# Kernel tuning notes

Hardware: AMD Instinct MI355X
Metric: run time of the kernel (lower is better)

Reference implementation:

```python
import jax, jax.numpy as jnp
import numpy as np

K = 64          # channels
B, D, H, W = 1, 64, 64, 64
W_STD = 1.0 / np.sqrt(K * 9)  # kaiming-like scale for 3x3 conv, fan_in = K*3*3


def _conv2d(x, w):
    # x: [B, C, A1, A2], w: [O, I, 3, 3]; SAME padding, stride 1, no bias
    return jax.lax.conv_general_dilated(
        x, w, window_strides=(1, 1), padding=((1, 1), (1, 1)),
        dimension_numbers=("NCHW", "OIHW", "NCHW"))


def _spatial_pass(x, w, tdim, reverse):
    # x: [B, C, D, H, W]; scan over tensor dim `tdim` (2=D, 3=H, 4=W).
    # Each slice (size-1 kernel along tdim in the original Conv3d) reduces to a
    # 2D 3x3 conv over the remaining two spatial axes.
    xs = jnp.moveaxis(x, tdim, 0)              # [L, B, C, A1, A2]
    if reverse:
        xs = xs[::-1]
    y0 = xs[0]

    def step(carry, sl):
        y = sl + jax.nn.relu(_conv2d(carry, w))
        return y, y

    _, ys = jax.lax.scan(step, y0, xs[1:])
    ys = jnp.concatenate([y0[None], ys], axis=0)
    if reverse:
        ys = ys[::-1]
    return jnp.moveaxis(ys, 0, tdim)


def setup_inputs() -> dict:
    key = jax.random.key(0)
    ks = jax.random.split(key, 7)
    x = jax.random.normal(ks[0], (B, K, D, H, W), dtype=jnp.float32)
    mk = lambda k: (jax.random.normal(k, (K, K, 3, 3), dtype=jnp.float32) * W_STD)
    # 2D equivalents of the six Conv3d weights (size-1 kernel axis squeezed):
    #   up_down/down_up:    (3,1,3) -> 3x3 over (D,W), scan over H
    #   left_right/right_left: (3,3,1) -> 3x3 over (D,H), scan over W
    #   front_back/back_front: (1,3,3) -> 3x3 over (H,W), scan over D
    return {
        "x": x,
        "w_ud": mk(ks[1]), "w_du": mk(ks[2]),
        "w_lr": mk(ks[3]), "w_rl": mk(ks[4]),
        "w_fb": mk(ks[5]), "w_bf": mk(ks[6]),
    }


def reference(x, w_ud, w_du, w_lr, w_rl, w_fb, w_bf):
    # dims = [1,1,2,2,0,0] in spatial coords -> tensor dims [3,3,4,4,2,2]
    x = _spatial_pass(x, w_ud, 3, False)
    x = _spatial_pass(x, w_du, 3, True)
    x = _spatial_pass(x, w_lr, 4, False)
    x = _spatial_pass(x, w_rl, 4, True)
    x = _spatial_pass(x, w_fb, 2, False)
    x = _spatial_pass(x, w_bf, 2, True)
    return x
```

## Files before the change

kernel.cpp:

```cpp
#include <hip/hip_runtime.h>

#define NELEM     16777216
#define CI_STRIDE 262144
#define WTP_PASS  36864
#define NFLAG     (6 * 256 * 16)
#define EX_PAR    262144

__device__ float    g_bufA[NELEM + 32];
__device__ float    g_bufB[NELEM + 32];
__device__ float    g_wtp[6 * WTP_PASS];
__device__ float    g_exch[2 * EX_PAR];
__device__ unsigned g_flags[NFLAG];

static __device__ __forceinline__ float ald(const float* p) {
    return __hip_atomic_load(p, __ATOMIC_RELAXED, __HIP_MEMORY_SCOPE_AGENT);
}
static __device__ __forceinline__ void ast(float* p, float v) {
    __hip_atomic_store(p, v, __ATOMIC_RELAXED, __HIP_MEMORY_SCOPE_AGENT);
}
static __device__ __forceinline__ float g4(const float4 v, int i) {
    switch (i) { case 0: return v.x; case 1: return v.y;
                 case 2: return v.z; default: return v.w; }
}

static __device__ __forceinline__ void kmap(int k, int& row, int& col) {
    if      (k < 4)  { row = 0;    col = k;      }
    else if (k < 8)  { row = 5;    col = k - 4;  }
    else if (k < 12) { row = k-7;  col = 0;      }
    else if (k < 16) { row = k-11; col = 5;      }
    else if (k < 18) { row = 0;    col = k - 12; }
    else             { row = 5;    col = k - 14; }
}

__global__ __launch_bounds__(256) void prep(
    const float* __restrict__ w0, const float* __restrict__ w1,
    const float* __restrict__ w2, const float* __restrict__ w3,
    const float* __restrict__ w4, const float* __restrict__ w5)
{
    int gid = blockIdx.x * 256 + threadIdx.x;
    if (gid < NFLAG) g_flags[gid] = 0;
    if (gid >= 6 * WTP_PASS) return;
    int p  = gid / WTP_PASS;
    int r  = gid % WTP_PASS;
    int co = r & 63;
    int q  = r >> 6;
    int kx = q % 3;
    int t2 = q / 3;
    int ky = t2 % 3;
    int ci = t2 / 3;
    const float* src = (p==0)?w0:(p==1)?w1:(p==2)?w2:(p==3)?w3:(p==4)?w4:w5;
    g_wtp[gid] = (p < 4) ? src[co*576 + ci*9 + ky*3 + kx]
                         : src[co*576 + ci*9 + kx*3 + ky];
}

__global__ __launch_bounds__(256) void transpose_hw(
    const float* __restrict__ in, float* __restrict__ out)
{
    __shared__ float t[64][65];
    const size_t base = (size_t)blockIdx.x * 4096;
    const int c  = threadIdx.x & 63;
    const int r4 = threadIdx.x >> 6;
#pragma unroll
    for (int r = 0; r < 16; ++r) {
        int a = r4 * 16 + r;
        t[a][c] = in[base + a * 64 + c];
    }
    __syncthreads();
#pragma unroll
    for (int r = 0; r < 16; ++r) {
        int bb = r4 * 16 + r;
        out[base + (size_t)bb * 64 + c] = t[c][bb];
    }
}

__global__ __launch_bounds__(512, 2) void pass_kernel(
    float* __restrict__ buf, const float* __restrict__ wtp,
    unsigned* __restrict__ flags, float* __restrict__ exch,
    int st, int su, int dir)
{
    __shared__ float lds[21504];
    float* rint = lds;
    float* ring = lds + 1024;
    float* red  = lds + 2560;

    const int tid  = threadIdx.x;
    const int lane = tid & 63;
    const int wv   = tid >> 6;
    const int B  = blockIdx.x;
    const int bu = ((B & 7) << 1) | ((B >> 7) & 1);
    const int bv = (B >> 3) & 15;
    const int b  = bu * 16 + bv;
    const int u0 = bu << 2, v0 = bv << 2;
    const int rr = wv >> 1, cc0 = (wv & 1) << 1;
    const int p0 = wv << 1;

    float W[8][3][3];
#pragma unroll
    for (int i = 0; i < 8; ++i)
#pragma unroll
        for (int ky = 0; ky < 3; ++ky)
#pragma unroll
            for (int kx = 0; kx < 3; ++kx)
                W[i][ky][kx] = wtp[(((wv*8 + i)*3 + ky)*3 + kx)*64 + lane];

    int nbr = -1;
    if (lane < 8) {
        int c  = lane + (lane >= 4 ? 1 : 0);
        int nu = bu + c/3 - 1, nv = bv + c%3 - 1;
        if (nu >= 0 && nu < 16 && nv >= 0 && nv < 16) nbr = (nu*16 + nv)*16;
    }

    int kk0=-1, kk1=-1, kk2=-1, so0=0, so1=0, so2=0;
#pragma unroll
    for (int j = 0; j < 3; ++j) {
        int k = wv + 8*j;
        if (k >= 20) continue;
        int row, col; kmap(k, row, col);
        int du = (row==0)?-1:(row==5)?1:0, dv = (col==0)?-1:(col==5)?1:0;
        int nu = bu + du, nv = bv + dv;
        if (nu < 0 || nu > 15 || nv < 0 || nv > 15) continue;
        int nb = nu*16 + nv;
        int lr = (row==0)?3:(row==5)?0:row-1;
        int lc = (col==0)?3:(col==5)?0:col-1;
        int so = (nb*16 + lr*4 + lc)*64 + lane;
        if      (j == 0) { kk0 = k; so0 = so; }
        else if (j == 1) { kk1 = k; so1 = so; }
        else             { kk2 = k; so2 = so; }
    }

    const int t0 = (dir > 0) ? 0 : 63;
    {
        const float2 iv = *(const float2*)(buf + (size_t)t0*st
              + (size_t)lane*CI_STRIDE + (size_t)(u0+rr)*su + (v0+cc0));
        *(float2*)&rint[(rr*64 + lane)*4 + cc0] = iv;
    }
#pragma unroll
    for (int j = 0; j < 3; ++j) {
        int k = wv + 8*j;
        if (k >= 20) continue;
        int row, col; kmap(k, row, col);
        int gu = u0 - 1 + row, gv = v0 - 1 + col;
        float v = 0.f;
        if (gu >= 0 && gu < 64 && gv >= 0 && gv < 64)
            v = buf[(size_t)t0*st + (size_t)lane*CI_STRIDE + (size_t)gu*su + gv];
        ring[lane*24 + k] = v;
    }
    __syncthreads();

    for (int s = 1; s <= 63; ++s) {
        const int t = (dir > 0) ? s : 63 - s;

        if (wv == 0 && s > 1) {
            const unsigned tgt = (unsigned)(s - 1);
            bool ok = (nbr < 0);
            if (!ok) ok = __hip_atomic_load(&flags[nbr], __ATOMIC_RELAXED,
                                            __HIP_MEMORY_SCOPE_AGENT) >= tgt;
            int spins = 0;
            while (!__all(ok) && spins < (1 << 22)) {
                __builtin_amdgcn_s_sleep(1);
                if (!ok) ok = __hip_atomic_load(&flags[nbr], __ATOMIC_RELAXED,
                                                __HIP_MEMORY_SCOPE_AGENT) >= tgt;
                ++spins;
            }
        }
        __syncthreads();

        const float2 xv = *(const float2*)(buf + (size_t)t*st
              + (size_t)lane*CI_STRIDE + (size_t)(u0+rr)*su + (v0+cc0));

        float c0 = 0.f, c1 = 0.f, c2 = 0.f;
        if (s > 1) {
            const float* xsrc = exch + (size_t)((s-1) & 1) * EX_PAR;
            if (kk0 >= 0) c0 = ald(xsrc + so0);
            if (kk1 >= 0) c1 = ald(xsrc + so1);
            if (kk2 >= 0) c2 = ald(xsrc + so2);
        }

        float acc[16];
#pragma unroll
        for (int p = 0; p < 16; ++p) acc[p] = 0.f;

#pragma unroll
        for (int i = 0; i < 8; ++i) {
            const int ci = wv*8 + i;
            const float4 R0 = *(const float4*)&rint[(0*64 + ci)*4];
            const float4 R1 = *(const float4*)&rint[(1*64 + ci)*4];
            const float4 R2 = *(const float4*)&rint[(2*64 + ci)*4];
            const float4 R3 = *(const float4*)&rint[(3*64 + ci)*4];
#pragma unroll
            for (int oi = 0; oi < 4; ++oi)
#pragma unroll
            for (int ky = 0; ky < 3; ++ky) {
                const int wr = oi + ky;
                if (wr < 1 || wr > 4) continue;
                const float4 Rw = (wr==1)?R0:(wr==2)?R1:(wr==3)?R2:R3;
#pragma unroll
                for (int oj = 0; oj < 4; ++oj)
#pragma unroll
                for (int kx = 0; kx < 3; ++kx) {
                    const int wc = oj + kx;
                    if (wc < 1 || wc > 4) continue;
                    acc[oi*4+oj] = fmaf(W[i][ky][kx], g4(Rw, wc-1), acc[oi*4+oj]);
                }
            }
        }

        if (s > 1) {
            if (kk0 >= 0) ring[lane*24 + kk0] = c0;
            if (kk1 >= 0) ring[lane*24 + kk1] = c1;
            if (kk2 >= 0) ring[lane*24 + kk2] = c2;
        }
        __syncthreads();

#pragma unroll
        for (int i = 0; i < 8; ++i) {
            const int ci = wv*8 + i;
            const float4 r0a = *(const float4*)&ring[ci*24 + 0];
            const float4 r5a = *(const float4*)&ring[ci*24 + 4];
            const float4 cl  = *(const float4*)&ring[ci*24 + 8];
            const float4 cr  = *(const float4*)&ring[ci*24 + 12];
            const float2 r0b = *(const float2*)&ring[ci*24 + 16];
            const float2 r5b = *(const float2*)&ring[ci*24 + 18];
#pragma unroll
            for (int oi = 0; oi < 4; ++oi)
#pragma unroll
            for (int ky = 0; ky < 3; ++ky) {
                const int wr = oi + ky;
#pragma unroll
                for (int oj = 0; oj < 4; ++oj)
#pragma unroll
                for (int kx = 0; kx < 3; ++kx) {
                    const int wc = oj + kx;
                    if (wr >= 1 && wr <= 4 && wc >= 1 && wc <= 4) continue;
                    float cell;
                    if      (wr == 0) cell = (wc < 4) ? g4(r0a, wc)
                                             : (wc == 4 ? r0b.x : r0b.y);
                    else if (wr == 5) cell = (wc < 4) ? g4(r5a, wc)
                                             : (wc == 4 ? r5b.x : r5b.y);
                    else if (wc == 0) cell = g4(cl, wr-1);
                    else              cell = g4(cr, wr-1);
                    acc[oi*4+oj] = fmaf(W[i][ky][kx], cell, acc[oi*4+oj]);
                }
            }
        }

#pragma unroll
        for (int p = 0; p < 16; ++p)
            red[(wv*16 + p)*64 + lane] = acc[p];
        __syncthreads();

        float s0 = 0.f, s1 = 0.f;
#pragma unroll
        for (int g = 0; g < 8; ++g) {
            s0 += red[(g*16 + p0    )*64 + lane];
            s1 += red[(g*16 + p0 + 1)*64 + lane];
        }
        const float o0 = xv.x + fmaxf(s0, 0.f);
        const float o1 = xv.y + fmaxf(s1, 0.f);

        *(float2*)(buf + (size_t)t*st + (size_t)lane*CI_STRIDE
                   + (size_t)(u0+rr)*su + (v0+cc0)) = make_float2(o0, o1);
        if (s < 63) {
            *(float2*)&rint[(rr*64 + lane)*4 + cc0] = make_float2(o0, o1);
            float* eb = exch + (size_t)(s & 1)*EX_PAR + b*1024;
            ast(eb + (p0    )*64 + lane, o0);
            ast(eb + (p0 + 1)*64 + lane, o1);
        }
        __syncthreads();

        if (s < 63 && tid == 0)
            __hip_atomic_store(&flags[b*16], (unsigned)s, __ATOMIC_RELAXED,
                               __HIP_MEMORY_SCOPE_AGENT);
    }
}

extern "C" void kernel_launch(void* const* d_in, const int* in_sizes, int n_in,
                              void* d_out, int out_size, void* d_ws, size_t ws_size,
                              hipStream_t stream)
{
    (void)in_sizes; (void)n_in; (void)out_size; (void)d_ws; (void)ws_size;
    const float* x = (const float*)d_in[0];
    float* out = (float*)d_out;

    void *pa, *pb, *pw, *pf, *pe;
    hipGetSymbolAddress(&pa, HIP_SYMBOL(g_bufA));
    hipGetSymbolAddress(&pb, HIP_SYMBOL(g_bufB));
    hipGetSymbolAddress(&pw, HIP_SYMBOL(g_wtp));
    hipGetSymbolAddress(&pf, HIP_SYMBOL(g_flags));
    hipGetSymbolAddress(&pe, HIP_SYMBOL(g_exch));
    float* A  = (float*)pa + 16;
    float* Bb = (float*)pb + 16;
    float* wtp = (float*)pw;
    unsigned* flags = (unsigned*)pf;
    float* exch = (float*)pe;

    prep<<<864, 256, 0, stream>>>(
        (const float*)d_in[1], (const float*)d_in[2], (const float*)d_in[3],
        (const float*)d_in[4], (const float*)d_in[5], (const float*)d_in[6]);

    hipMemcpyAsync(A, x, (size_t)NELEM * sizeof(float),
                   hipMemcpyDeviceToDevice, stream);

    pass_kernel<<<256, 512, 0, stream>>>(A, wtp + 0*WTP_PASS, flags + 0*4096, exch, 64, 4096, +1);
    pass_kernel<<<256, 512, 0, stream>>>(A, wtp + 1*WTP_PASS, flags + 1*4096, exch, 64, 4096, -1);

    transpose_hw<<<4096, 256, 0, stream>>>(A, Bb);

    pass_kernel<<<256, 512, 0, stream>>>(Bb, wtp + 2*WTP_PASS, flags + 2*4096, exch, 64, 4096, +1);
    pass_kernel<<<256, 512, 0, stream>>>(Bb, wtp + 3*WTP_PASS, flags + 3*4096, exch, 64, 4096, -1);
    pass_kernel<<<256, 512, 0, stream>>>(Bb, wtp + 4*WTP_PASS, flags + 4*4096, exch, 4096, 64, +1);
    pass_kernel<<<256, 512, 0, stream>>>(Bb, wtp + 5*WTP_PASS, flags + 5*4096, exch, 4096, 64, -1);

    transpose_hw<<<4096, 256, 0, stream>>>(Bb, out);
}
```

Baseline: 2.490 ms.

## Switch to channels-last layout and double pass-kernel block size to 1024 threads

Replaces the channel-major layout with a channels-last buffer, so each of the 64 channels at a spatial point is contiguous. The input memcpy and mid transpose become one relayout kernel at entry and one at exit, and the pass kernel takes three strides so one layout serves all six scan directions. Pass-kernel blocks grow from 512 to 1024 threads, with each wave computing half the output rows of its channel group. The intent is fully coalesced per-step loads and stores and more parallelism per step. The cost is more LDS reduction traffic per step and higher register and occupancy pressure from launch_bounds(1024,4).

```diff
diff --git a/kernel.cpp b/kernel.cpp
--- a/kernel.cpp
+++ b/kernel.cpp
@@ -1,13 +1,11 @@
 #include <hip/hip_runtime.h>
 
 #define NELEM     16777216
-#define CI_STRIDE 262144
 #define WTP_PASS  36864
 #define NFLAG     (6 * 256 * 16)
 #define EX_PAR    262144
 
-__device__ float    g_bufA[NELEM + 32];
-__device__ float    g_bufB[NELEM + 32];
+__device__ float    g_bufA[NELEM];
 __device__ float    g_wtp[6 * WTP_PASS];
 __device__ float    g_exch[2 * EX_PAR];
 __device__ unsigned g_flags[NFLAG];
@@ -49,34 +47,53 @@
     int ky = t2 % 3;
     int ci = t2 / 3;
     const float* src = (p==0)?w0:(p==1)?w1:(p==2)?w2:(p==3)?w3:(p==4)?w4:w5;
-    g_wtp[gid] = (p < 4) ? src[co*576 + ci*9 + ky*3 + kx]
-                         : src[co*576 + ci*9 + kx*3 + ky];
-}
-
-__global__ __launch_bounds__(256) void transpose_hw(
+    g_wtp[gid] = src[co*576 + ci*9 + ky*3 + kx];
+}
+
+__global__ __launch_bounds__(256) void relayout_in(
     const float* __restrict__ in, float* __restrict__ out)
 {
     __shared__ float t[64][65];
-    const size_t base = (size_t)blockIdx.x * 4096;
+    const int o = blockIdx.x;
     const int c  = threadIdx.x & 63;
     const int r4 = threadIdx.x >> 6;
 #pragma unroll
     for (int r = 0; r < 16; ++r) {
-        int a = r4 * 16 + r;
-        t[a][c] = in[base + a * 64 + c];
+        int ch = r4 * 16 + r;
+        t[ch][c] = in[(size_t)ch * 262144 + o * 64 + c];
     }
     __syncthreads();
 #pragma unroll
     for (int r = 0; r < 16; ++r) {
-        int bb = r4 * 16 + r;
-        out[base + (size_t)bb * 64 + c] = t[c][bb];
-    }
-}
-
-__global__ __launch_bounds__(512, 2) void pass_kernel(
+        int j = r4 * 16 + r;
+        out[((size_t)o * 64 + j) * 64 + c] = t[c][j];
+    }
+}
+
+__global__ __launch_bounds__(256) void relayout_out(
+    const float* __restrict__ in, float* __restrict__ out)
+{
+    __shared__ float t[64][65];
+    const int o = blockIdx.x;
+    const int c  = threadIdx.x & 63;
+    const int r4 = threadIdx.x >> 6;
+#pragma unroll
+    for (int r = 0; r < 16; ++r) {
+        int j = r4 * 16 + r;
+        t[j][c] = in[((size_t)o * 64 + j) * 64 + c];
+    }
+    __syncthreads();
+#pragma unroll
+    for (int r = 0; r < 16; ++r) {
+        int ch = r4 * 16 + r;
+        out[(size_t)ch * 262144 + o * 64 + c] = t[c][ch];
+    }
+}
+
+__global__ __launch_bounds__(1024, 4) void pass_kernel(
     float* __restrict__ buf, const float* __restrict__ wtp,
     unsigned* __restrict__ flags, float* __restrict__ exch,
-    int st, int su, int dir)
+    int stp, int sup, int svp, int dir)
 {
     __shared__ float lds[21504];
     float* rint = lds;
@@ -86,13 +103,15 @@
     const int tid  = threadIdx.x;
     const int lane = tid & 63;
     const int wv   = tid >> 6;
+    const int g    = wv & 7;
+    const int h    = wv >> 3;
+    const int oiB  = 2 * h;
     const int B  = blockIdx.x;
     const int bu = ((B & 7) << 1) | ((B >> 7) & 1);
     const int bv = (B >> 3) & 15;
     const int b  = bu * 16 + bv;
     const int u0 = bu << 2, v0 = bv << 2;
-    const int rr = wv >> 1, cc0 = (wv & 1) << 1;
-    const int p0 = wv << 1;
+    const int row = wv >> 2, col = wv & 3;
 
     float W[8][3][3];
 #pragma unroll
@@ -101,7 +120,7 @@
         for (int ky = 0; ky < 3; ++ky)
 #pragma unroll
             for (int kx = 0; kx < 3; ++kx)
-                W[i][ky][kx] = wtp[(((wv*8 + i)*3 + ky)*3 + kx)*64 + lane];
+                W[i][ky][kx] = wtp[(((g*8 + i)*3 + ky)*3 + kx)*64 + lane];
 
     int nbr = -1;
     if (lane < 8) {
@@ -110,39 +129,34 @@
         if (nu >= 0 && nu < 16 && nv >= 0 && nv < 16) nbr = (nu*16 + nv)*16;
     }
 
-    int kk0=-1, kk1=-1, kk2=-1, so0=0, so1=0, so2=0;
-#pragma unroll
-    for (int j = 0; j < 3; ++j) {
-        int k = wv + 8*j;
+    int kkA = -1, soA = 0, kkB = -1, soB = 0;
+#pragma unroll
+    for (int j = 0; j < 2; ++j) {
+        int k = (j == 0) ? wv : (wv < 4 ? 16 + wv : 99);
         if (k >= 20) continue;
-        int row, col; kmap(k, row, col);
-        int du = (row==0)?-1:(row==5)?1:0, dv = (col==0)?-1:(col==5)?1:0;
+        int kr, kc; kmap(k, kr, kc);
+        int du = (kr==0)?-1:(kr==5)?1:0, dv = (kc==0)?-1:(kc==5)?1:0;
         int nu = bu + du, nv = bv + dv;
         if (nu < 0 || nu > 15 || nv < 0 || nv > 15) continue;
         int nb = nu*16 + nv;
-        int lr = (row==0)?3:(row==5)?0:row-1;
-        int lc = (col==0)?3:(col==5)?0:col-1;
+        int lr = (kr==0)?3:(kr==5)?0:kr-1;
+        int lc = (kc==0)?3:(kc==5)?0:kc-1;
         int so = (nb*16 + lr*4 + lc)*64 + lane;
-        if      (j == 0) { kk0 = k; so0 = so; }
-        else if (j == 1) { kk1 = k; so1 = so; }
-        else             { kk2 = k; so2 = so; }
+        if (j == 0) { kkA = k; soA = so; } else { kkB = k; soB = so; }
     }
 
     const int t0 = (dir > 0) ? 0 : 63;
-    {
-        const float2 iv = *(const float2*)(buf + (size_t)t0*st
-              + (size_t)lane*CI_STRIDE + (size_t)(u0+rr)*su + (v0+cc0));
-        *(float2*)&rint[(rr*64 + lane)*4 + cc0] = iv;
-    }
-#pragma unroll
-    for (int j = 0; j < 3; ++j) {
-        int k = wv + 8*j;
+    rint[(row*64 + lane)*4 + col] =
+        buf[((size_t)(t0*stp + (u0+row)*sup + (v0+col)*svp) << 6) + lane];
+#pragma unroll
+    for (int j = 0; j < 2; ++j) {
+        int k = (j == 0) ? wv : (wv < 4 ? 16 + wv : 99);
         if (k >= 20) continue;
-        int row, col; kmap(k, row, col);
-        int gu = u0 - 1 + row, gv = v0 - 1 + col;
+        int kr, kc; kmap(k, kr, kc);
+        int gu = u0 - 1 + kr, gv = v0 - 1 + kc;
         float v = 0.f;
         if (gu >= 0 && gu < 64 && gv >= 0 && gv < 64)
-            v = buf[(size_t)t0*st + (size_t)lane*CI_STRIDE + (size_t)gu*su + gv];
+            v = buf[((size_t)(t0*stp + gu*sup + gv*svp) << 6) + lane];
         ring[lane*24 + k] = v;
     }
     __syncthreads();
@@ -165,56 +179,59 @@
         }
         __syncthreads();
 
-        const float2 xv = *(const float2*)(buf + (size_t)t*st
-              + (size_t)lane*CI_STRIDE + (size_t)(u0+rr)*su + (v0+cc0));
-
-        float c0 = 0.f, c1 = 0.f, c2 = 0.f;
+        const size_t oaddr =
+            ((size_t)(t*stp + (u0+row)*sup + (v0+col)*svp) << 6) + lane;
+        const float xv = buf[oaddr];
+
+        float cA = 0.f, cB = 0.f;
         if (s > 1) {
             const float* xsrc = exch + (size_t)((s-1) & 1) * EX_PAR;
-            if (kk0 >= 0) c0 = ald(xsrc + so0);
-            if (kk1 >= 0) c1 = ald(xsrc + so1);
-            if (kk2 >= 0) c2 = ald(xsrc + so2);
-        }
-
-        float acc[16];
-#pragma unroll
-        for (int p = 0; p < 16; ++p) acc[p] = 0.f;
-
+            if (kkA >= 0) cA = ald(xsrc + soA);
+            if (kkB >= 0) cB = ald(xsrc + soB);
+        }
+
+        float acc[8];
+#pragma unroll
+        for (int p = 0; p < 8; ++p) acc[p] = 0.f;
+
+        const int rowStart = h;
 #pragma unroll
         for (int i = 0; i < 8; ++i) {
-            const int ci = wv*8 + i;
-            const float4 R0 = *(const float4*)&rint[(0*64 + ci)*4];
-            const float4 R1 = *(const float4*)&rint[(1*64 + ci)*4];
-            const float4 R2 = *(const float4*)&rint[(2*64 + ci)*4];
-            const float4 R3 = *(const float4*)&rint[(3*64 + ci)*4];
-#pragma unroll
-            for (int oi = 0; oi < 4; ++oi)
-#pragma unroll
-            for (int ky = 0; ky < 3; ++ky) {
-                const int wr = oi + ky;
-                if (wr < 1 || wr > 4) continue;
-                const float4 Rw = (wr==1)?R0:(wr==2)?R1:(wr==3)?R2:R3;
-#pragma unroll
-                for (int oj = 0; oj < 4; ++oj)
-#pragma unroll
-                for (int kx = 0; kx < 3; ++kx) {
-                    const int wc = oj + kx;
-                    if (wc < 1 || wc > 4) continue;
-                    acc[oi*4+oj] = fmaf(W[i][ky][kx], g4(Rw, wc-1), acc[oi*4+oj]);
+            const int ci = g*8 + i;
+            const float4 R0 = *(const float4*)&rint[((rowStart+0)*64 + ci)*4];
+            const float4 R1 = *(const float4*)&rint[((rowStart+1)*64 + ci)*4];
+            const float4 R2 = *(const float4*)&rint[((rowStart+2)*64 + ci)*4];
+#pragma unroll
+            for (int lp = 0; lp < 2; ++lp) {
+                const int oi = oiB + lp;
+#pragma unroll
+                for (int ky = 0; ky < 3; ++ky) {
+                    const int wr = oi + ky;
+                    if (wr < 1 || wr > 4) continue;
+                    const int ri = wr - 1 - rowStart;
+                    const float4 Rw = (ri == 0) ? R0 : (ri == 1) ? R1 : R2;
+#pragma unroll
+                    for (int oj = 0; oj < 4; ++oj)
+#pragma unroll
+                    for (int kx = 0; kx < 3; ++kx) {
+                        const int wc = oj + kx;
+                        if (wc < 1 || wc > 4) continue;
+                        acc[lp*4+oj] = fmaf(W[i][ky][kx], g4(Rw, wc-1),
+                                            acc[lp*4+oj]);
+                    }
                 }
             }
         }
 
         if (s > 1) {
-            if (kk0 >= 0) ring[lane*24 + kk0] = c0;
-            if (kk1 >= 0) ring[lane*24 + kk1] = c1;
-            if (kk2 >= 0) ring[lane*24 + kk2] = c2;
+            if (kkA >= 0) ring[lane*24 + kkA] = cA;
+            if (kkB >= 0) ring[lane*24 + kkB] = cB;
         }
         __syncthreads();
 
 #pragma unroll
         for (int i = 0; i < 8; ++i) {
-            const int ci = wv*8 + i;
+            const int ci = g*8 + i;
             const float4 r0a = *(const float4*)&ring[ci*24 + 0];
             const float4 r5a = *(const float4*)&ring[ci*24 + 4];
             const float4 cl  = *(const float4*)&ring[ci*24 + 8];
@@ -222,49 +239,45 @@
             const float2 r0b = *(const float2*)&ring[ci*24 + 16];
             const float2 r5b = *(const float2*)&ring[ci*24 + 18];
 #pragma unroll
-            for (int oi = 0; oi < 4; ++oi)
-#pragma unroll
-            for (int ky = 0; ky < 3; ++ky) {
-                const int wr = oi + ky;
-#pragma unroll
-                for (int oj = 0; oj < 4; ++oj)
-#pragma unroll
-                for (int kx = 0; kx < 3; ++kx) {
-                    const int wc = oj + kx;
-                    if (wr >= 1 && wr <= 4 && wc >= 1 && wc <= 4) continue;
-                    float cell;
-                    if      (wr == 0) cell = (wc < 4) ? g4(r0a, wc)
-                                             : (wc == 4 ? r0b.x : r0b.y);
-                    else if (wr == 5) cell = (wc < 4) ? g4(r5a, wc)
-                                             : (wc == 4 ? r5b.x : r5b.y);
-                    else if (wc == 0) cell = g4(cl, wr-1);
-                    else              cell = g4(cr, wr-1);
-                    acc[oi*4+oj] = fmaf(W[i][ky][kx], cell, acc[oi*4+oj]);
+            for (int lp = 0; lp < 2; ++lp) {
+                const int oi = oiB + lp;
+#pragma unroll
+                for (int ky = 0; ky < 3; ++ky) {
+                    const int wr = oi + ky;
+#pragma unroll
+                    for (int oj = 0; oj < 4; ++oj)
+#pragma unroll
+                    for (int kx = 0; kx < 3; ++kx) {
+                        const int wc = oj + kx;
+                        if (wr >= 1 && wr <= 4 && wc >= 1 && wc <= 4) continue;
+                        float cell;
+                        if      (wr == 0) cell = (wc < 4) ? g4(r0a, wc)
+                                                 : (wc == 4 ? r0b.x : r0b.y);
+                        else if (wr == 5) cell = (wc < 4) ? g4(r5a, wc)
+                                                 : (wc == 4 ? r5b.x : r5b.y);
+                        else if (wc == 0) cell = g4(cl, wr-1);
+                        else              cell = g4(cr, wr-1);
+                        acc[lp*4+oj] = fmaf(W[i][ky][kx], cell, acc[lp*4+oj]);
+                    }
                 }
             }
         }
 
 #pragma unroll
-        for (int p = 0; p < 16; ++p)
-            red[(wv*16 + p)*64 + lane] = acc[p];
+        for (int p = 0; p < 8; ++p)
+            red[(g*16 + 8*h + p)*64 + lane] = acc[p];
         __syncthreads();
 
-        float s0 = 0.f, s1 = 0.f;
-#pragma unroll
-        for (int g = 0; g < 8; ++g) {
-            s0 += red[(g*16 + p0    )*64 + lane];
-            s1 += red[(g*16 + p0 + 1)*64 + lane];
-        }
-        const float o0 = xv.x + fmaxf(s0, 0.f);
-        const float o1 = xv.y + fmaxf(s1, 0.f);
-
-        *(float2*)(buf + (size_t)t*st + (size_t)lane*CI_STRIDE
-                   + (size_t)(u0+rr)*su + (v0+cc0)) = make_float2(o0, o1);
+        float sum = 0.f;
+#pragma unroll
+        for (int g2 = 0; g2 < 8; ++g2)
+            sum += red[(g2*16 + wv)*64 + lane];
+        const float o = xv + fmaxf(sum, 0.f);
+
+        buf[oaddr] = o;
         if (s < 63) {
-            *(float2*)&rint[(rr*64 + lane)*4 + cc0] = make_float2(o0, o1);
-            float* eb = exch + (size_t)(s & 1)*EX_PAR + b*1024;
-            ast(eb + (p0    )*64 + lane, o0);
-            ast(eb + (p0 + 1)*64 + lane, o1);
+            rint[(row*64 + lane)*4 + col] = o;
+            ast(exch + (size_t)(s & 1)*EX_PAR + b*1024 + wv*64 + lane, o);
         }
         __syncthreads();
 
@@ -282,14 +295,12 @@
     const float* x = (const float*)d_in[0];
     float* out = (float*)d_out;
 
-    void *pa, *pb, *pw, *pf, *pe;
+    void *pa, *pw, *pf, *pe;
     hipGetSymbolAddress(&pa, HIP_SYMBOL(g_bufA));
-    hipGetSymbolAddress(&pb, HIP_SYMBOL(g_bufB));
     hipGetSymbolAddress(&pw, HIP_SYMBOL(g_wtp));
     hipGetSymbolAddress(&pf, HIP_SYMBOL(g_flags));
     hipGetSymbolAddress(&pe, HIP_SYMBOL(g_exch));
-    float* A  = (float*)pa + 16;
-    float* Bb = (float*)pb + 16;
+    float* A = (float*)pa;
     float* wtp = (float*)pw;
     unsigned* flags = (unsigned*)pf;
     float* exch = (float*)pe;
@@ -298,18 +309,14 @@
         (const float*)d_in[1], (const float*)d_in[2], (const float*)d_in[3],
         (const float*)d_in[4], (const float*)d_in[5], (const float*)d_in[6]);
 
-    hipMemcpyAsync(A, x, (size_t)NELEM * sizeof(float),
-                   hipMemcpyDeviceToDevice, stream);
-
-    pass_kernel<<<256, 512, 0, stream>>>(A, wtp + 0*WTP_PASS, flags + 0*4096, exch, 64, 4096, +1);
-    pass_kernel<<<256, 512, 0, stream>>>(A, wtp + 1*WTP_PASS, flags + 1*4096, exch, 64, 4096, -1);
-
-    transpose_hw<<<4096, 256, 0, stream>>>(A, Bb);
-
-    pass_kernel<<<256, 512, 0, stream>>>(Bb, wtp + 2*WTP_PASS, flags + 2*4096, exch, 64, 4096, +1);
-    pass_kernel<<<256, 512, 0, stream>>>(Bb, wtp + 3*WTP_PASS, flags + 3*4096, exch, 64, 4096, -1);
-    pass_kernel<<<256, 512, 0, stream>>>(Bb, wtp + 4*WTP_PASS, flags + 4*4096, exch, 4096, 64, +1);
-    pass_kernel<<<256, 512, 0, stream>>>(Bb, wtp + 5*WTP_PASS, flags + 5*4096, exch, 4096, 64, -1);
-
-    transpose_hw<<<4096, 256, 0, stream>>>(Bb, out);
-}
+    relayout_in<<<4096, 256, 0, stream>>>(x, A);
+
+    pass_kernel<<<256, 1024, 0, stream>>>(A, wtp + 0*WTP_PASS, flags + 0*4096, exch, 64, 4096, 1, +1);
+    pass_kernel<<<256, 1024, 0, stream>>>(A, wtp + 1*WTP_PASS, flags + 1*4096, exch, 64, 4096, 1, -1);
+    pass_kernel<<<256, 1024, 0, stream>>>(A, wtp + 2*WTP_PASS, flags + 2*4096, exch, 1, 4096, 64, +1);
+    pass_kernel<<<256, 1024, 0, stream>>>(A, wtp + 3*WTP_PASS, flags + 3*4096, exch, 1, 4096, 64, -1);
+    pass_kernel<<<256, 1024, 0, stream>>>(A, wtp + 4*WTP_PASS, flags + 4*4096, exch, 4096, 64, 1, +1);
+    pass_kernel<<<256, 1024, 0, stream>>>(A, wtp + 5*WTP_PASS, flags + 5*4096, exch, 4096, 64, 1, -1);
+
+    relayout_out<<<4096, 256, 0, stream>>>(A, out);
+}
```

Result: slower. 8.376 ms (+236.5%).
